# Kernel tuning notes

Measured on AMD Instinct MI355X. Metric: run time of the kernel, lower is better.

Reference implementation:

```python
import jax, jax.numpy as jnp
import numpy as np

N = 10000   # total nodes (hits) across events
K = 16      # n_neighbours (excluding self)
F = 64      # input feature dim
H = 128     # hidden width (hard-coded in module)
BIG = 1e9

def _selu(x):
    return jax.nn.selu(x)

def _glorot(key, shape):
    fan_in, fan_out = shape
    s = jnp.sqrt(2.0 / (fan_in + fan_out)).astype(jnp.float32)
    return jax.random.normal(key, shape, dtype=jnp.float32) * s

def setup_inputs() -> dict:
    key = jax.random.key(0)
    ks = jax.random.split(key, 10)
    h = jax.random.normal(ks[0], (N, F), dtype=jnp.float32)
    coords = jax.random.normal(ks[1], (N, 3), dtype=jnp.float32)
    row_splits = jnp.array([0, N // 2, N], dtype=jnp.int32)
    return {
        'h': h, 'coords': coords, 'row_splits': row_splits,
        'W_e1': _glorot(ks[2], (2 * F + 1, H)), 'b_e1': jnp.zeros((H,), jnp.float32),
        'W_e2': _glorot(ks[3], (H, H)), 'b_e2': jnp.zeros((H,), jnp.float32),
        'W_c1': _glorot(ks[4], (H, H)), 'b_c1': jnp.zeros((H,), jnp.float32),
        'W_c2': _glorot(ks[5], (H, 1)), 'b_c2': jnp.zeros((1,), jnp.float32),
        'W_n1': _glorot(ks[6], (H + F, H)), 'b_n1': jnp.zeros((H,), jnp.float32),
        'W_n2': _glorot(ks[7], (H, H)), 'b_n2': jnp.zeros((H,), jnp.float32),
    }

def _knn(coords, row_splits):
    # segment id per node from row_splits (constant)
    n = coords.shape[0]
    seg = jnp.searchsorted(row_splits, jnp.arange(n), side='right') - 1
    nrm = jnp.sum(coords * coords, axis=1)                      # [N]
    d2 = nrm[:, None] + nrm[None, :] - 2.0 * (coords @ coords.T)
    d2 = jnp.maximum(d2, 0.0)
    same = seg[:, None] == seg[None, :]
    d2 = jnp.where(same, d2, BIG)
    negd, idx = jax.lax.top_k(-d2, K + 1)                       # includes self (dist 0)
    dist = jnp.maximum(-negd, 0.0)                              # [N, K+1]
    return idx, dist

def reference(h, coords, row_splits, W_e1, b_e1, W_e2, b_e2, W_c1, b_c1, W_c2, b_c2, W_n1, b_n1, W_n2, b_n2):
    idx, dist = _knn(coords, row_splits)                        # [N,K+1]
    nidx = idx[:, 1:]                                           # [N,K]
    d = dist[:, 1:]                                             # [N,K]
    coord_diff = coords[:, None, :] - coords[idx[:, 1:]]        # [N,K,3]

    hg = h[idx]                                                 # SelectWithDefault gather [N,K+1,F]
    h_self = hg[:, 0, :]                                        # [N,F]
    h_node = jnp.broadcast_to(h_self[:, None, :], (h.shape[0], K, F)).reshape(-1, F)
    h_neig = hg[:, 1:, :].reshape(-1, F)
    radial0 = d.reshape(-1, 1)

    e = jnp.concatenate([radial0, h_node, h_neig], axis=1)      # [N*K, 2F+1]
    e = _selu(e @ W_e1 + b_e1)
    e = _selu(e @ W_e2 + b_e2)                                  # [N*K, H]

    c = _selu(e @ W_c1 + b_c1)
    w = (c @ W_c2 + b_c2).reshape(-1, K, 1)                     # [N,K,1]
    trans = jnp.mean(coord_diff * w, axis=1)                    # [N,3]
    coords_new = coords + trans

    e_sum = e.reshape(-1, K, H).sum(axis=1)                     # [N,H]
    agg = jnp.concatenate([e_sum, h_self], axis=1)              # [N,H+F]
    out = _selu(agg @ W_n1 + b_n1) @ W_n2 + b_n2                # [N,H]
    return out, coords_new, nidx, d
```

## Files before the change

kernel.cpp:

```cpp
#include <hip/hip_runtime.h>
#include <cstdint>

#define KNB 16
#define FDIM 64
#define HDIM 128
#define SA 130
#define SW 65
#define CMAXW 80

typedef unsigned long long ull;
typedef _Float16 f16x8 __attribute__((ext_vector_type(8)));
typedef float    f32x16 __attribute__((ext_vector_type(16)));

__device__ __forceinline__ float selu_f(float x){
    const float a = 1.6732632423543772f, s = 1.0507009873554805f;
    return x > 0.f ? s * x : s * a * expm1f(x);
}

__device__ __forceinline__ unsigned int pack2(float a, float b){
    union { _Float16 h[2]; unsigned int u; } t;
    t.h[0] = (_Float16)a; t.h[1] = (_Float16)b;
    return t.u;
}

__device__ __forceinline__ f16x8 ldfrag(const unsigned int* p, unsigned int di){
    union { unsigned int u[4]; f16x8 v; } t;
    t.u[0] = p[di]; t.u[1] = p[di+1]; t.u[2] = p[di+2]; t.u[3] = p[di+3];
    return t.v;
}

template<int CTRL>
__device__ __forceinline__ unsigned int dppmin_u32(unsigned int v){
    unsigned int t = (unsigned int)__builtin_amdgcn_update_dpp(
        -1, (int)v, CTRL, 0xF, 0xF, false);
    return t < v ? t : v;
}
__device__ __forceinline__ unsigned int wave_min_u32(unsigned int v){
    v = dppmin_u32<0x111>(v);
    v = dppmin_u32<0x112>(v);
    v = dppmin_u32<0x114>(v);
    v = dppmin_u32<0x118>(v);
    v = dppmin_u32<0x142>(v);
    v = dppmin_u32<0x143>(v);
    return (unsigned int)__builtin_amdgcn_readlane((int)v, 63);
}

__global__ __launch_bounds__(256) void conv_kernel(
    const float* __restrict__ We1, const float* __restrict__ We2,
    const float* __restrict__ Wc1, _Float16* __restrict__ WT)
{
    int id = blockIdx.x * 256 + threadIdx.x;
    int m  = id >> 14;
    int r  = id & 16383;
    int nn = (r >> 7) & 127;
    int k  = r & 127;
    float v;
    if (m == 0)      v = We1[(k + 1) * 128 + nn];
    else if (m == 1) v = We2[k * 128 + nn];
    else             v = Wc1[k * 128 + nn];
    WT[m * 16384 + nn * 128 + k] = (_Float16)v;
}

__global__ __launch_bounds__(256) void knn_kernel(
    const float* __restrict__ coords,
    const int* __restrict__ row_splits, int nseg, int n,
    int* __restrict__ nidx, float* __restrict__ ndist, int* __restrict__ idx0,
    float* __restrict__ out_nidx, float* __restrict__ out_d)
{
    const int lane = threadIdx.x & 63;
    const int wid  = threadIdx.x >> 6;
    const int i    = blockIdx.x * 4 + wid;
    if (i >= n) return;

    int lo = 0, hi = n;
    for (int s = 0; s < nseg; ++s){
        int a = row_splits[s], b = row_splits[s+1];
        if (i >= a && i < b){ lo = a; hi = b; }
    }

    const float cx = coords[3*i], cy = coords[3*i+1], cz = coords[3*i+2];
    const float nrmi = __fadd_rn(__fadd_rn(__fmul_rn(cx,cx), __fmul_rn(cy,cy)), __fmul_rn(cz,cz));

    const int jbase = lo + lane;
    const float FINF = __uint_as_float(0x7f800000u);

    ull m1 = ~0ull, m2 = ~0ull, m3 = ~0ull;
    {
        const float* cp = coords + (size_t)3 * jbase;
        for (int c = 0; c < CMAXW; ++c){
            int j = jbase + c*64;
            float dv = FINF;
            if (j < hi){
                float x = cp[0], y = cp[1], z = cp[2];
                float nrmj = __fadd_rn(__fadd_rn(__fmul_rn(x,x), __fmul_rn(y,y)), __fmul_rn(z,z));
                float dot  = __fadd_rn(__fadd_rn(__fmul_rn(cx,x), __fmul_rn(cy,y)), __fmul_rn(cz,z));
                float d2 = __fsub_rn(__fadd_rn(nrmi, nrmj), __fmul_rn(2.0f, dot));
                dv = fmaxf(d2, 0.0f);
            }
            cp += 192;
            ull kk = (((ull)__float_as_uint(dv)) << 32) | (unsigned int)j;
            ull n1 = kk < m1 ? kk : m1;
            ull t1 = kk < m1 ? m1 : kk;
            ull n2 = t1 < m2 ? t1 : m2;
            ull t2 = t1 < m2 ? m2 : t1;
            ull n3 = t2 < m3 ? t2 : m3;
            m1 = n1; m2 = n2; m3 = n3;
        }
    }
    int vcnt = 3;

    for (int r = 0; r < KNB + 1; ++r){
        unsigned int h32 = (unsigned int)(m1 >> 32);
        unsigned int l32 = (unsigned int)m1;
        unsigned int wmd = wave_min_u32(h32);
        unsigned int jm  = (h32 == wmd) ? l32 : 0xFFFFFFFFu;
        unsigned int wmj = wave_min_u32(jm);

        bool own = (h32 == wmd) && (l32 == wmj);
        bool need = false;
        if (own){
            int   j  = (int)wmj;
            float dv = __uint_as_float(wmd);
            if (r == 0){
                idx0[i] = j;
            } else {
                int rr = r - 1;
                nidx[i*KNB + rr]     = j;
                ndist[i*KNB + rr]    = dv;
                out_nidx[i*KNB + rr] = (float)j;
                out_d[i*KNB + rr]    = dv;
            }
            m1 = m2; m2 = m3; m3 = ~0ull;
            need = (--vcnt == 0);
        }

        if (__ballot((int)need)){
            if (need){
                ull b = (((ull)wmd) << 32) | wmj;
                m1 = m2 = m3 = ~0ull;
                const float* cq = coords + (size_t)3 * jbase;
                for (int c = 0; c < CMAXW; ++c){
                    int j = jbase + c*64;
                    float dv = FINF;
                    if (j < hi){
                        float x = cq[0], y = cq[1], z = cq[2];
                        float nrmj = __fadd_rn(__fadd_rn(__fmul_rn(x,x), __fmul_rn(y,y)), __fmul_rn(z,z));
                        float dot  = __fadd_rn(__fadd_rn(__fmul_rn(cx,x), __fmul_rn(cy,y)), __fmul_rn(cz,z));
                        float d2 = __fsub_rn(__fadd_rn(nrmi, nrmj), __fmul_rn(2.0f, dot));
                        dv = fmaxf(d2, 0.0f);
                    }
                    cq += 192;
                    ull kk = (((ull)__float_as_uint(dv)) << 32) | (unsigned int)j;
                    kk = kk > b ? kk : ~0ull;
                    ull n1 = kk < m1 ? kk : m1;
                    ull t1 = kk < m1 ? m1 : kk;
                    ull n2 = t1 < m2 ? t1 : m2;
                    ull t2 = t1 < m2 ? m2 : t1;
                    ull n3 = t2 < m3 ? t2 : m3;
                    m1 = n1; m2 = n2; m3 = n3;
                }
                vcnt = 3;
            }
        }
    }
}

__global__ __launch_bounds__(256, 3) void egcn_node_kernel(
    const float* __restrict__ h, const float* __restrict__ coords,
    const int* __restrict__ nidx, const float* __restrict__ ndist,
    const int* __restrict__ idx0, const _Float16* __restrict__ WTg,
    const float* __restrict__ W_e1, const float* __restrict__ b_e1,
    const float* __restrict__ b_e2, const float* __restrict__ b_c1,
    const float* __restrict__ W_c2, const float* __restrict__ b_c2,
    float* __restrict__ aggout, float* __restrict__ out_coords, int n)
{
    __shared__ _Float16 Act[64 * SA];
    __shared__ unsigned int wt[128 * SW];
    __shared__ float agg[4][HDIM];
    __shared__ float dls[64];
    __shared__ int   nb[64];
    __shared__ int   j0s[4];
    __shared__ float wedge[64];
    __shared__ float wedgep[2][64];

    const int g0  = blockIdx.x * 4;
    const int tid = threadIdx.x;
    const int lane = tid & 63, wid = tid >> 6;
    const int ln31 = lane & 31, grp = lane >> 5;
    const int rt  = wid & 1;
    const int ct0 = (wid >> 1) * 2;

    if (tid < 64){
        int e = min(g0*KNB + tid, n*KNB - 1);
        nb[tid]  = nidx[e];
        dls[tid] = ndist[e];
    }
    if (tid < 4) j0s[tid] = idx0[min(g0 + tid, n - 1)];
    __syncthreads();

    unsigned int* actd = (unsigned int*)Act;

    {
        int r = tid >> 2, q = tid & 3, f0 = q * 16;
        const float* hs = h + (size_t)j0s[r >> 4] * FDIM + f0;
        const float* hn = h + (size_t)nb[r] * FDIM + f0;
        unsigned int ds = (unsigned int)(r * SA + f0) >> 1;
        unsigned int dn = (unsigned int)(r * SA + FDIM + f0) >> 1;
        #pragma unroll
        for (int j = 0; j < 8; ++j){
            actd[ds + j] = pack2(hs[2*j], hs[2*j+1]);
            actd[dn + j] = pack2(hn[2*j], hn[2*j+1]);
        }
    }
    {
        int nr = tid >> 1, kh = (tid & 1) * 64;
        const uint4* src = (const uint4*)(WTg + nr * 128 + kh);
        unsigned int* dst = wt + nr * SW + (tid & 1) * 32;
        #pragma unroll
        for (int j = 0; j < 8; ++j){
            uint4 x = src[j];
            dst[j*4+0]=x.x; dst[j*4+1]=x.y; dst[j*4+2]=x.z; dst[j*4+3]=x.w;
        }
    }
    __syncthreads();

    const unsigned int aBase  = (unsigned int)(rt*32 + ln31) * SW + grp*4;
    const unsigned int bBase0 = (unsigned int)(ct0*32 + ln31) * SW + grp*4;
    const unsigned int bBase1 = (unsigned int)((ct0+1)*32 + ln31) * SW + grp*4;

    auto gemm2 = [&](f32x16& A0, f32x16& A1){
        #pragma unroll
        for (int ks = 0; ks < 8; ++ks){
            const unsigned int off = ks * 8;
            f16x8 af  = ldfrag(actd, aBase + off);
            f16x8 bf0 = ldfrag(wt, bBase0 + off);
            f16x8 bf1 = ldfrag(wt, bBase1 + off);
            A0 = __builtin_amdgcn_mfma_f32_32x32x16_f16(af, bf0, A0, 0, 0, 0);
            A1 = __builtin_amdgcn_mfma_f32_32x32x16_f16(af, bf1, A1, 0, 0, 0);
        }
    };
    auto stage_wt = [&](const _Float16* Wg){
        int nr = tid >> 1, kh = (tid & 1) * 64;
        const uint4* src = (const uint4*)(Wg + nr * 128 + kh);
        unsigned int* dst = wt + nr * SW + (tid & 1) * 32;
        #pragma unroll
        for (int j = 0; j < 8; ++j){
            uint4 x = src[j];
            dst[j*4+0]=x.x; dst[j*4+1]=x.y; dst[j*4+2]=x.z; dst[j*4+3]=x.w;
        }
    };

    {
        float w0a = W_e1[ct0*32 + ln31], w0b = W_e1[(ct0+1)*32 + ln31];
        float bza = b_e1[ct0*32 + ln31], bzb = b_e1[(ct0+1)*32 + ln31];
        f32x16 a0, a1;
        #pragma unroll
        for (int reg = 0; reg < 16; ++reg){
            int row32 = (reg&3) + 8*(reg>>2) + 4*grp;
            float dv = dls[rt*32 + row32];
            a0[reg] = fmaf(dv, w0a, bza);
            a1[reg] = fmaf(dv, w0b, bzb);
        }
        gemm2(a0, a1);
        __syncthreads();
        #pragma unroll
        for (int reg = 0; reg < 16; ++reg){
            int row = rt*32 + (reg&3) + 8*(reg>>2) + 4*grp;
            Act[row*SA + ct0*32 + ln31]     = (_Float16)selu_f(a0[reg]);
            Act[row*SA + (ct0+1)*32 + ln31] = (_Float16)selu_f(a1[reg]);
        }
        stage_wt(WTg + 16384);
        __syncthreads();
    }

    {
        float bza = b_e2[ct0*32 + ln31], bzb = b_e2[(ct0+1)*32 + ln31];
        f32x16 a0, a1;
        #pragma unroll
        for (int reg = 0; reg < 16; ++reg){ a0[reg] = bza; a1[reg] = bzb; }
        gemm2(a0, a1);
        __syncthreads();
        float ev0[16], ev1[16];
        float slo0 = 0.f, shi0 = 0.f, slo1 = 0.f, shi1 = 0.f;
        #pragma unroll
        for (int reg = 0; reg < 16; ++reg){
            ev0[reg] = selu_f(a0[reg]);
            ev1[reg] = selu_f(a1[reg]);
            if (reg < 8){ slo0 += ev0[reg]; slo1 += ev1[reg]; }
            else        { shi0 += ev0[reg]; shi1 += ev1[reg]; }
        }
        slo0 += __shfl_xor(slo0, 32, 64);
        shi0 += __shfl_xor(shi0, 32, 64);
        slo1 += __shfl_xor(slo1, 32, 64);
        shi1 += __shfl_xor(shi1, 32, 64);
        if (grp == 0){
            agg[rt*2+0][ct0*32 + ln31]     = slo0;
            agg[rt*2+1][ct0*32 + ln31]     = shi0;
            agg[rt*2+0][(ct0+1)*32 + ln31] = slo1;
            agg[rt*2+1][(ct0+1)*32 + ln31] = shi1;
        }
        #pragma unroll
        for (int reg = 0; reg < 16; ++reg){
            int row = rt*32 + (reg&3) + 8*(reg>>2) + 4*grp;
            Act[row*SA + ct0*32 + ln31]     = (_Float16)ev0[reg];
            Act[row*SA + (ct0+1)*32 + ln31] = (_Float16)ev1[reg];
        }
        stage_wt(WTg + 2*16384);
        __syncthreads();
    }

    {
        float bza = b_c1[ct0*32 + ln31], bzb = b_c1[(ct0+1)*32 + ln31];
        f32x16 a0, a1;
        #pragma unroll
        for (int reg = 0; reg < 16; ++reg){ a0[reg] = bza; a1[reg] = bzb; }
        gemm2(a0, a1);
        __syncthreads();
        float wca = W_c2[ct0*32 + ln31], wcb = W_c2[(ct0+1)*32 + ln31];
        float p[16];
        #pragma unroll
        for (int reg = 0; reg < 16; ++reg)
            p[reg] = selu_f(a0[reg]) * wca + selu_f(a1[reg]) * wcb;
        #pragma unroll
        for (int msk = 16; msk > 0; msk >>= 1){
            #pragma unroll
            for (int reg = 0; reg < 16; ++reg)
                p[reg] += __shfl_xor(p[reg], msk, 64);
        }
        if (ln31 == 0){
            #pragma unroll
            for (int reg = 0; reg < 16; ++reg){
                int row = rt*32 + (reg&3) + 8*(reg>>2) + 4*grp;
                wedgep[wid>>1][row] = p[reg];
            }
        }
        __syncthreads();
    }

    if (tid < 64) wedge[tid] = b_c2[0] + wedgep[0][tid] + wedgep[1][tid];
    __syncthreads();

    if (tid < 12){
        int nd = tid / 3, c = tid - nd*3;
        int gi = min(g0 + nd, n - 1);
        float ci = coords[3*gi + c];
        float s = 0.f;
        #pragma unroll
        for (int k = 0; k < KNB; ++k){
            int e = nd*KNB + k;
            s += (ci - coords[3*nb[e] + c]) * wedge[e];
        }
        if (g0 + nd < n) out_coords[3*gi + c] = ci + s * (1.0f/KNB);
    }

    for (int s = tid; s < 4*192; s += 256){
        int nd = s / 192, c = s - nd*192;
        if (g0 + nd < n){
            float v = (c < HDIM) ? agg[nd][c]
                                 : h[(size_t)j0s[nd]*FDIM + (c - HDIM)];
            aggout[(size_t)(g0 + nd)*192 + c] = v;
        }
    }
}

#define NMB 16
__global__ __launch_bounds__(256) void node_mlp_kernel(
    const float* __restrict__ aggin,
    const float* __restrict__ W_n1, const float* __restrict__ b_n1,
    const float* __restrict__ W_n2, const float* __restrict__ b_n2,
    float* __restrict__ out, int n)
{
    __shared__ __attribute__((aligned(16))) float sinT[192][20];
    __shared__ float part[2][NMB][HDIM];

    const int g0  = blockIdx.x * NMB;
    const int tid = threadIdx.x;
    const int o    = tid & 127;
    const int half = tid >> 7;

    for (int s = tid; s < NMB*192; s += 256){
        size_t gidx = (size_t)g0*192 + s;
        size_t lim  = (size_t)n*192 - 1;
        float v = aggin[gidx < lim ? gidx : lim];
        int nd = s / 192, in = s - nd*192;
        sinT[in][nd] = v;
    }
    __syncthreads();

    {
        float a[NMB];
        #pragma unroll
        for (int d = 0; d < NMB; ++d) a[d] = 0.f;
        int in0 = half * 96;
        for (int in = in0; in < in0 + 96; ++in){
            float w = W_n1[in*HDIM + o];
            const float4* sp = (const float4*)&sinT[in][0];
            float4 v0 = sp[0], v1 = sp[1], v2 = sp[2], v3 = sp[3];
            a[0]  = fmaf(v0.x, w, a[0]);  a[1]  = fmaf(v0.y, w, a[1]);
            a[2]  = fmaf(v0.z, w, a[2]);  a[3]  = fmaf(v0.w, w, a[3]);
            a[4]  = fmaf(v1.x, w, a[4]);  a[5]  = fmaf(v1.y, w, a[5]);
            a[6]  = fmaf(v1.z, w, a[6]);  a[7]  = fmaf(v1.w, w, a[7]);
            a[8]  = fmaf(v2.x, w, a[8]);  a[9]  = fmaf(v2.y, w, a[9]);
            a[10] = fmaf(v2.z, w, a[10]); a[11] = fmaf(v2.w, w, a[11]);
            a[12] = fmaf(v3.x, w, a[12]); a[13] = fmaf(v3.y, w, a[13]);
            a[14] = fmaf(v3.z, w, a[14]); a[15] = fmaf(v3.w, w, a[15]);
        }
        #pragma unroll
        for (int d = 0; d < NMB; ++d) part[half][d][o] = a[d];
    }
    __syncthreads();

    for (int s = tid; s < NMB*HDIM; s += 256){
        int nd = s >> 7, o2 = s & 127;
        sinT[o2][nd] = selu_f(part[0][nd][o2] + part[1][nd][o2] + b_n1[o2]);
    }
    __syncthreads();

    {
        float a[NMB];
        #pragma unroll
        for (int d = 0; d < NMB; ++d) a[d] = 0.f;
        int in0 = half * 64;
        for (int in = in0; in < in0 + 64; ++in){
            float w = W_n2[in*HDIM + o];
            const float4* sp = (const float4*)&sinT[in][0];
            float4 v0 = sp[0], v1 = sp[1], v2 = sp[2], v3 = sp[3];
            a[0]  = fmaf(v0.x, w, a[0]);  a[1]  = fmaf(v0.y, w, a[1]);
            a[2]  = fmaf(v0.z, w, a[2]);  a[3]  = fmaf(v0.w, w, a[3]);
            a[4]  = fmaf(v1.x, w, a[4]);  a[5]  = fmaf(v1.y, w, a[5]);
            a[6]  = fmaf(v1.z, w, a[6]);  a[7]  = fmaf(v1.w, w, a[7]);
            a[8]  = fmaf(v2.x, w, a[8]);  a[9]  = fmaf(v2.y, w, a[9]);
            a[10] = fmaf(v2.z, w, a[10]); a[11] = fmaf(v2.w, w, a[11]);
            a[12] = fmaf(v3.x, w, a[12]); a[13] = fmaf(v3.y, w, a[13]);
            a[14] = fmaf(v3.z, w, a[14]); a[15] = fmaf(v3.w, w, a[15]);
        }
        #pragma unroll
        for (int d = 0; d < NMB; ++d) part[half][d][o] = a[d];
    }
    __syncthreads();

    for (int s = tid; s < NMB*HDIM; s += 256){
        int nd = s >> 7, o2 = s & 127;
        if (g0 + nd < n)
            out[(size_t)(g0 + nd)*HDIM + o2] =
                part[0][nd][o2] + part[1][nd][o2] + b_n2[o2];
    }
}

extern "C" void kernel_launch(void* const* d_in, const int* in_sizes, int n_in,
                              void* d_out, int out_size, void* d_ws, size_t ws_size,
                              hipStream_t stream)
{
    const float* h          = (const float*)d_in[0];
    const float* coords     = (const float*)d_in[1];
    const int*   row_splits = (const int*)  d_in[2];
    const float* W_e1 = (const float*)d_in[3];
    const float* b_e1 = (const float*)d_in[4];
    const float* W_e2 = (const float*)d_in[5];
    const float* b_e2 = (const float*)d_in[6];
    const float* W_c1 = (const float*)d_in[7];
    const float* b_c1 = (const float*)d_in[8];
    const float* W_c2 = (const float*)d_in[9];
    const float* b_c2 = (const float*)d_in[10];
    const float* W_n1 = (const float*)d_in[11];
    const float* b_n1 = (const float*)d_in[12];
    const float* W_n2 = (const float*)d_in[13];
    const float* b_n2 = (const float*)d_in[14];

    const int n    = in_sizes[0] / FDIM;
    const int nseg = in_sizes[2] - 1;

    float* out        = (float*)d_out;
    float* out_coords = out + (size_t)n * HDIM;
    float* out_nidx   = out_coords + (size_t)n * 3;
    float* out_d      = out_nidx + (size_t)n * KNB;

    int*       nidx_i = (int*)d_ws;
    float*     ndist  = (float*)(nidx_i + (size_t)n * KNB);
    int*       idx0   = (int*)(ndist + (size_t)n * KNB);
    _Float16*  WT     = (_Float16*)(idx0 + (size_t)n);
    float*     aggbuf = (float*)(WT + 3 * 16384);

    conv_kernel<<<192, 256, 0, stream>>>(W_e1, W_e2, W_c1, WT);

    knn_kernel<<<(n + 3) / 4, 256, 0, stream>>>(coords, row_splits, nseg, n,
                                                nidx_i, ndist, idx0, out_nidx, out_d);

    egcn_node_kernel<<<(n + 3) / 4, 256, 0, stream>>>(
        h, coords, nidx_i, ndist, idx0, WT,
        W_e1, b_e1, b_e2, b_c1, W_c2, b_c2,
        aggbuf, out_coords, n);

    node_mlp_kernel<<<(n + NMB - 1) / NMB, 256, 0, stream>>>(
        aggbuf, W_n1, b_n1, W_n2, b_n2, out, n);
}
```

Measured before the change: 285.7 us.

## Pack coords as float4, unroll KNN scan, double edge tile per block

A new pre-pass packs coordinates together with their squared norm into float4, so the KNN scan does one vector load per candidate and skips recomputing the norm. The scan's first pass is unrolled by four to overlap loads. The edge MLP kernel now handles 8 nodes (128 edge rows) per block, with each wave computing all four 32-column tiles. Fragment loads use 128-bit LDS reads with padded strides, and selu switches to __expf. Shared memory per block grows and occupancy drops to 2 blocks per CU, and the fast exp may slightly change precision.

After: 257.7 us. 1.11x faster.

```diff
diff --git a/kernel.cpp b/kernel.cpp
--- a/kernel.cpp
+++ b/kernel.cpp
@@ -4,8 +4,11 @@
 #define KNB 16
 #define FDIM 64
 #define HDIM 128
-#define SA 130
-#define SW 65
+#define NPB 8
+#define ROWS 128
+#define SA 136
+#define SAD 68
+#define SW 68
 #define CMAXW 80
 
 typedef unsigned long long ull;
@@ -14,7 +17,7 @@
 
 __device__ __forceinline__ float selu_f(float x){
     const float a = 1.6732632423543772f, s = 1.0507009873554805f;
-    return x > 0.f ? s * x : s * a * expm1f(x);
+    return x > 0.f ? s * x : s * a * (__expf(x) - 1.0f);
 }
 
 __device__ __forceinline__ unsigned int pack2(float a, float b){
@@ -23,9 +26,9 @@
     return t.u;
 }
 
-__device__ __forceinline__ f16x8 ldfrag(const unsigned int* p, unsigned int di){
-    union { unsigned int u[4]; f16x8 v; } t;
-    t.u[0] = p[di]; t.u[1] = p[di+1]; t.u[2] = p[di+2]; t.u[3] = p[di+3];
+__device__ __forceinline__ f16x8 ldfrag4(const unsigned int* p, unsigned int di){
+    union { uint4 q; f16x8 v; } t;
+    t.q = *(const uint4*)(p + di);
     return t.v;
 }
 
@@ -61,8 +64,19 @@
     WT[m * 16384 + nn * 128 + k] = (_Float16)v;
 }
 
+__global__ __launch_bounds__(256) void pack4_kernel(
+    const float* __restrict__ coords, float4* __restrict__ c4, int n)
+{
+    int i = blockIdx.x * 256 + threadIdx.x;
+    if (i < n){
+        float x = coords[3*i], y = coords[3*i+1], z = coords[3*i+2];
+        float nrm = __fadd_rn(__fadd_rn(__fmul_rn(x,x), __fmul_rn(y,y)), __fmul_rn(z,z));
+        c4[i] = make_float4(x, y, z, nrm);
+    }
+}
+
 __global__ __launch_bounds__(256) void knn_kernel(
-    const float* __restrict__ coords,
+    const float4* __restrict__ c4,
     const int* __restrict__ row_splits, int nseg, int n,
     int* __restrict__ nidx, float* __restrict__ ndist, int* __restrict__ idx0,
     float* __restrict__ out_nidx, float* __restrict__ out_d)
@@ -78,34 +92,42 @@
         if (i >= a && i < b){ lo = a; hi = b; }
     }
 
-    const float cx = coords[3*i], cy = coords[3*i+1], cz = coords[3*i+2];
-    const float nrmi = __fadd_rn(__fadd_rn(__fmul_rn(cx,cx), __fmul_rn(cy,cy)), __fmul_rn(cz,cz));
+    const float4 ci = c4[i];
+    const float cx = ci.x, cy = ci.y, cz = ci.z, nrmi = ci.w;
 
     const int jbase = lo + lane;
     const float FINF = __uint_as_float(0x7f800000u);
 
     ull m1 = ~0ull, m2 = ~0ull, m3 = ~0ull;
-    {
-        const float* cp = coords + (size_t)3 * jbase;
-        for (int c = 0; c < CMAXW; ++c){
-            int j = jbase + c*64;
-            float dv = FINF;
-            if (j < hi){
-                float x = cp[0], y = cp[1], z = cp[2];
-                float nrmj = __fadd_rn(__fadd_rn(__fmul_rn(x,x), __fmul_rn(y,y)), __fmul_rn(z,z));
-                float dot  = __fadd_rn(__fadd_rn(__fmul_rn(cx,x), __fmul_rn(cy,y)), __fmul_rn(cz,z));
-                float d2 = __fsub_rn(__fadd_rn(nrmi, nrmj), __fmul_rn(2.0f, dot));
-                dv = fmaxf(d2, 0.0f);
-            }
-            cp += 192;
-            ull kk = (((ull)__float_as_uint(dv)) << 32) | (unsigned int)j;
-            ull n1 = kk < m1 ? kk : m1;
-            ull t1 = kk < m1 ? m1 : kk;
-            ull n2 = t1 < m2 ? t1 : m2;
-            ull t2 = t1 < m2 ? m2 : t1;
-            ull n3 = t2 < m3 ? t2 : m3;
-            m1 = n1; m2 = n2; m3 = n3;
-        }
+
+    #define D2_OF(v) __fsub_rn(__fadd_rn(nrmi, (v).w), __fmul_rn(2.0f, \
+        __fadd_rn(__fadd_rn(__fmul_rn(cx,(v).x), __fmul_rn(cy,(v).y)), __fmul_rn(cz,(v).z))))
+    #define INS(kk) { \
+        ull n1 = (kk) < m1 ? (kk) : m1; \
+        ull t1 = (kk) < m1 ? m1 : (kk); \
+        ull n2 = t1 < m2 ? t1 : m2; \
+        ull t2 = t1 < m2 ? m2 : t1; \
+        ull n3 = t2 < m3 ? t2 : m3; \
+        m1 = n1; m2 = n2; m3 = n3; }
+
+    for (int c0 = 0; c0 < CMAXW; c0 += 4){
+        int j0 = jbase + (c0+0)*64;
+        int j1 = jbase + (c0+1)*64;
+        int j2 = jbase + (c0+2)*64;
+        int j3 = jbase + (c0+3)*64;
+        float4 v0 = c4[min(j0, hi-1)];
+        float4 v1 = c4[min(j1, hi-1)];
+        float4 v2 = c4[min(j2, hi-1)];
+        float4 v3 = c4[min(j3, hi-1)];
+        float d0 = (j0 < hi) ? fmaxf(D2_OF(v0), 0.0f) : FINF;
+        float d1 = (j1 < hi) ? fmaxf(D2_OF(v1), 0.0f) : FINF;
+        float d2 = (j2 < hi) ? fmaxf(D2_OF(v2), 0.0f) : FINF;
+        float d3 = (j3 < hi) ? fmaxf(D2_OF(v3), 0.0f) : FINF;
+        ull k0 = (((ull)__float_as_uint(d0)) << 32) | (unsigned int)j0;
+        ull k1 = (((ull)__float_as_uint(d1)) << 32) | (unsigned int)j1;
+        ull k2 = (((ull)__float_as_uint(d2)) << 32) | (unsigned int)j2;
+        ull k3 = (((ull)__float_as_uint(d3)) << 32) | (unsigned int)j3;
+        INS(k0) INS(k1) INS(k2) INS(k3)
     }
     int vcnt = 3;
 
@@ -138,34 +160,23 @@
             if (need){
                 ull b = (((ull)wmd) << 32) | wmj;
                 m1 = m2 = m3 = ~0ull;
-                const float* cq = coords + (size_t)3 * jbase;
                 for (int c = 0; c < CMAXW; ++c){
                     int j = jbase + c*64;
-                    float dv = FINF;
-                    if (j < hi){
-                        float x = cq[0], y = cq[1], z = cq[2];
-                        float nrmj = __fadd_rn(__fadd_rn(__fmul_rn(x,x), __fmul_rn(y,y)), __fmul_rn(z,z));
-                        float dot  = __fadd_rn(__fadd_rn(__fmul_rn(cx,x), __fmul_rn(cy,y)), __fmul_rn(cz,z));
-                        float d2 = __fsub_rn(__fadd_rn(nrmi, nrmj), __fmul_rn(2.0f, dot));
-                        dv = fmaxf(d2, 0.0f);
-                    }
-                    cq += 192;
+                    float4 v = c4[min(j, hi-1)];
+                    float dv = (j < hi) ? fmaxf(D2_OF(v), 0.0f) : FINF;
                     ull kk = (((ull)__float_as_uint(dv)) << 32) | (unsigned int)j;
                     kk = kk > b ? kk : ~0ull;
-                    ull n1 = kk < m1 ? kk : m1;
-                    ull t1 = kk < m1 ? m1 : kk;
-                    ull n2 = t1 < m2 ? t1 : m2;
-                    ull t2 = t1 < m2 ? m2 : t1;
-                    ull n3 = t2 < m3 ? t2 : m3;
-                    m1 = n1; m2 = n2; m3 = n3;
+                    INS(kk)
                 }
                 vcnt = 3;
             }
         }
     }
-}
-
-__global__ __launch_bounds__(256, 3) void egcn_node_kernel(
+    #undef INS
+    #undef D2_OF
+}
+
+__global__ __launch_bounds__(256, 2) void egcn_node_kernel(
     const float* __restrict__ h, const float* __restrict__ coords,
     const int* __restrict__ nidx, const float* __restrict__ ndist,
     const int* __restrict__ idx0, const _Float16* __restrict__ WTg,
@@ -174,153 +185,165 @@
     const float* __restrict__ W_c2, const float* __restrict__ b_c2,
     float* __restrict__ aggout, float* __restrict__ out_coords, int n)
 {
-    __shared__ _Float16 Act[64 * SA];
-    __shared__ unsigned int wt[128 * SW];
-    __shared__ float agg[4][HDIM];
-    __shared__ float dls[64];
-    __shared__ int   nb[64];
-    __shared__ int   j0s[4];
-    __shared__ float wedge[64];
-    __shared__ float wedgep[2][64];
-
-    const int g0  = blockIdx.x * 4;
+    __shared__ __attribute__((aligned(16))) _Float16 Act[ROWS * SA];
+    __shared__ __attribute__((aligned(16))) unsigned int wt[ROWS * SW];
+    __shared__ float agg[NPB][HDIM];
+    __shared__ float dls[ROWS];
+    __shared__ int   nb[ROWS];
+    __shared__ int   j0s[NPB];
+    __shared__ float wedge[ROWS];
+
+    const int g0  = blockIdx.x * NPB;
     const int tid = threadIdx.x;
     const int lane = tid & 63, wid = tid >> 6;
     const int ln31 = lane & 31, grp = lane >> 5;
-    const int rt  = wid & 1;
-    const int ct0 = (wid >> 1) * 2;
-
-    if (tid < 64){
+    const int rt  = wid;
+
+    if (tid < ROWS){
         int e = min(g0*KNB + tid, n*KNB - 1);
         nb[tid]  = nidx[e];
         dls[tid] = ndist[e];
     }
-    if (tid < 4) j0s[tid] = idx0[min(g0 + tid, n - 1)];
+    if (tid < NPB) j0s[tid] = idx0[min(g0 + tid, n - 1)];
     __syncthreads();
 
     unsigned int* actd = (unsigned int*)Act;
 
     {
-        int r = tid >> 2, q = tid & 3, f0 = q * 16;
-        const float* hs = h + (size_t)j0s[r >> 4] * FDIM + f0;
-        const float* hn = h + (size_t)nb[r] * FDIM + f0;
-        unsigned int ds = (unsigned int)(r * SA + f0) >> 1;
-        unsigned int dn = (unsigned int)(r * SA + FDIM + f0) >> 1;
-        #pragma unroll
-        for (int j = 0; j < 8; ++j){
-            actd[ds + j] = pack2(hs[2*j], hs[2*j+1]);
-            actd[dn + j] = pack2(hn[2*j], hn[2*j+1]);
-        }
-    }
-    {
-        int nr = tid >> 1, kh = (tid & 1) * 64;
-        const uint4* src = (const uint4*)(WTg + nr * 128 + kh);
-        unsigned int* dst = wt + nr * SW + (tid & 1) * 32;
-        #pragma unroll
-        for (int j = 0; j < 8; ++j){
-            uint4 x = src[j];
-            dst[j*4+0]=x.x; dst[j*4+1]=x.y; dst[j*4+2]=x.z; dst[j*4+3]=x.w;
-        }
-    }
+        int r = tid >> 1, half = tid & 1;
+        const float4* hs = (const float4*)(h + (size_t)j0s[r >> 4] * FDIM + half*32);
+        const float4* hn = (const float4*)(h + (size_t)nb[r] * FDIM + half*32);
+        unsigned int base = (unsigned int)r * SAD + half*16;
+        uint4 buf[4];
+        #pragma unroll
+        for (int q = 0; q < 4; ++q){
+            float4 a = hs[2*q], b = hs[2*q+1];
+            buf[q].x = pack2(a.x,a.y); buf[q].y = pack2(a.z,a.w);
+            buf[q].z = pack2(b.x,b.y); buf[q].w = pack2(b.z,b.w);
+        }
+        #pragma unroll
+        for (int q = 0; q < 4; ++q) *(uint4*)(actd + base + 4*q) = buf[q];
+        #pragma unroll
+        for (int q = 0; q < 4; ++q){
+            float4 a = hn[2*q], b = hn[2*q+1];
+            buf[q].x = pack2(a.x,a.y); buf[q].y = pack2(a.z,a.w);
+            buf[q].z = pack2(b.x,b.y); buf[q].w = pack2(b.z,b.w);
+        }
+        #pragma unroll
+        for (int q = 0; q < 4; ++q) *(uint4*)(actd + base + 32 + 4*q) = buf[q];
+    }
+    auto stage_wt = [&](const _Float16* Wg){
+        int nr = tid >> 1, half = tid & 1;
+        const uint4* src = (const uint4*)(Wg + nr * 128 + half*64);
+        uint4* dst = (uint4*)(wt + nr * SW + half*32);
+        #pragma unroll
+        for (int q = 0; q < 8; ++q) dst[q] = src[q];
+    };
+    stage_wt(WTg);
     __syncthreads();
 
-    const unsigned int aBase  = (unsigned int)(rt*32 + ln31) * SW + grp*4;
-    const unsigned int bBase0 = (unsigned int)(ct0*32 + ln31) * SW + grp*4;
-    const unsigned int bBase1 = (unsigned int)((ct0+1)*32 + ln31) * SW + grp*4;
-
-    auto gemm2 = [&](f32x16& A0, f32x16& A1){
+    const unsigned int aBase = (unsigned int)(rt*32 + ln31) * SAD + grp*4;
+    const unsigned int bB0   = (unsigned int)(ln31      ) * SW + grp*4;
+    const unsigned int bB1   = (unsigned int)(32  + ln31) * SW + grp*4;
+    const unsigned int bB2   = (unsigned int)(64  + ln31) * SW + grp*4;
+    const unsigned int bB3   = (unsigned int)(96  + ln31) * SW + grp*4;
+
+    auto gemm4 = [&](f32x16& A0, f32x16& A1, f32x16& A2, f32x16& A3){
         #pragma unroll
         for (int ks = 0; ks < 8; ++ks){
             const unsigned int off = ks * 8;
-            f16x8 af  = ldfrag(actd, aBase + off);
-            f16x8 bf0 = ldfrag(wt, bBase0 + off);
-            f16x8 bf1 = ldfrag(wt, bBase1 + off);
-            A0 = __builtin_amdgcn_mfma_f32_32x32x16_f16(af, bf0, A0, 0, 0, 0);
-            A1 = __builtin_amdgcn_mfma_f32_32x32x16_f16(af, bf1, A1, 0, 0, 0);
+            f16x8 af = ldfrag4(actd, aBase + off);
+            A0 = __builtin_amdgcn_mfma_f32_32x32x16_f16(af, ldfrag4(wt, bB0 + off), A0, 0, 0, 0);
+            A1 = __builtin_amdgcn_mfma_f32_32x32x16_f16(af, ldfrag4(wt, bB1 + off), A1, 0, 0, 0);
+            A2 = __builtin_amdgcn_mfma_f32_32x32x16_f16(af, ldfrag4(wt, bB2 + off), A2, 0, 0, 0);
+            A3 = __builtin_amdgcn_mfma_f32_32x32x16_f16(af, ldfrag4(wt, bB3 + off), A3, 0, 0, 0);
         }
     };
-    auto stage_wt = [&](const _Float16* Wg){
-        int nr = tid >> 1, kh = (tid & 1) * 64;
-        const uint4* src = (const uint4*)(Wg + nr * 128 + kh);
-        unsigned int* dst = wt + nr * SW + (tid & 1) * 32;
-        #pragma unroll
-        for (int j = 0; j < 8; ++j){
-            uint4 x = src[j];
-            dst[j*4+0]=x.x; dst[j*4+1]=x.y; dst[j*4+2]=x.z; dst[j*4+3]=x.w;
-        }
-    };
+    #define ROW_OF(reg) (rt*32 + ((reg)&3) + 8*((reg)>>2) + 4*grp)
 
     {
-        float w0a = W_e1[ct0*32 + ln31], w0b = W_e1[(ct0+1)*32 + ln31];
-        float bza = b_e1[ct0*32 + ln31], bzb = b_e1[(ct0+1)*32 + ln31];
-        f32x16 a0, a1;
+        float w00 = W_e1[ln31],      w01 = W_e1[32+ln31];
+        float w02 = W_e1[64+ln31],   w03 = W_e1[96+ln31];
+        float bz0 = b_e1[ln31],      bz1 = b_e1[32+ln31];
+        float bz2 = b_e1[64+ln31],   bz3 = b_e1[96+ln31];
+        f32x16 a0, a1, a2, a3;
         #pragma unroll
         for (int reg = 0; reg < 16; ++reg){
-            int row32 = (reg&3) + 8*(reg>>2) + 4*grp;
-            float dv = dls[rt*32 + row32];
-            a0[reg] = fmaf(dv, w0a, bza);
-            a1[reg] = fmaf(dv, w0b, bzb);
-        }
-        gemm2(a0, a1);
+            float dv = dls[ROW_OF(reg)];
+            a0[reg] = fmaf(dv, w00, bz0);
+            a1[reg] = fmaf(dv, w01, bz1);
+            a2[reg] = fmaf(dv, w02, bz2);
+            a3[reg] = fmaf(dv, w03, bz3);
+        }
+        gemm4(a0, a1, a2, a3);
         __syncthreads();
         #pragma unroll
         for (int reg = 0; reg < 16; ++reg){
-            int row = rt*32 + (reg&3) + 8*(reg>>2) + 4*grp;
-            Act[row*SA + ct0*32 + ln31]     = (_Float16)selu_f(a0[reg]);
-            Act[row*SA + (ct0+1)*32 + ln31] = (_Float16)selu_f(a1[reg]);
+            int row = ROW_OF(reg);
+            Act[row*SA + ln31]      = (_Float16)selu_f(a0[reg]);
+            Act[row*SA + 32 + ln31] = (_Float16)selu_f(a1[reg]);
+            Act[row*SA + 64 + ln31] = (_Float16)selu_f(a2[reg]);
+            Act[row*SA + 96 + ln31] = (_Float16)selu_f(a3[reg]);
         }
         stage_wt(WTg + 16384);
         __syncthreads();
     }
 
     {
-        float bza = b_e2[ct0*32 + ln31], bzb = b_e2[(ct0+1)*32 + ln31];
-        f32x16 a0, a1;
-        #pragma unroll
-        for (int reg = 0; reg < 16; ++reg){ a0[reg] = bza; a1[reg] = bzb; }
-        gemm2(a0, a1);
+        float bz0 = b_e2[ln31],    bz1 = b_e2[32+ln31];
+        float bz2 = b_e2[64+ln31], bz3 = b_e2[96+ln31];
+        f32x16 a0, a1, a2, a3;
+        #pragma unroll
+        for (int reg = 0; reg < 16; ++reg){ a0[reg]=bz0; a1[reg]=bz1; a2[reg]=bz2; a3[reg]=bz3; }
+        gemm4(a0, a1, a2, a3);
         __syncthreads();
-        float ev0[16], ev1[16];
-        float slo0 = 0.f, shi0 = 0.f, slo1 = 0.f, shi1 = 0.f;
+        float e0[16], e1v[16], e2v[16], e3[16];
+        float sl0=0.f, sh0=0.f, sl1=0.f, sh1=0.f, sl2=0.f, sh2=0.f, sl3=0.f, sh3=0.f;
         #pragma unroll
         for (int reg = 0; reg < 16; ++reg){
-            ev0[reg] = selu_f(a0[reg]);
-            ev1[reg] = selu_f(a1[reg]);
-            if (reg < 8){ slo0 += ev0[reg]; slo1 += ev1[reg]; }
-            else        { shi0 += ev0[reg]; shi1 += ev1[reg]; }
-        }
-        slo0 += __shfl_xor(slo0, 32, 64);
-        shi0 += __shfl_xor(shi0, 32, 64);
-        slo1 += __shfl_xor(slo1, 32, 64);
-        shi1 += __shfl_xor(shi1, 32, 64);
+            e0[reg]=selu_f(a0[reg]); e1v[reg]=selu_f(a1[reg]);
+            e2v[reg]=selu_f(a2[reg]); e3[reg]=selu_f(a3[reg]);
+            if (reg < 8){ sl0+=e0[reg]; sl1+=e1v[reg]; sl2+=e2v[reg]; sl3+=e3[reg]; }
+            else        { sh0+=e0[reg]; sh1+=e1v[reg]; sh2+=e2v[reg]; sh3+=e3[reg]; }
+        }
+        sl0 += __shfl_xor(sl0, 32, 64);  sh0 += __shfl_xor(sh0, 32, 64);
+        sl1 += __shfl_xor(sl1, 32, 64);  sh1 += __shfl_xor(sh1, 32, 64);
+        sl2 += __shfl_xor(sl2, 32, 64);  sh2 += __shfl_xor(sh2, 32, 64);
+        sl3 += __shfl_xor(sl3, 32, 64);  sh3 += __shfl_xor(sh3, 32, 64);
         if (grp == 0){
-            agg[rt*2+0][ct0*32 + ln31]     = slo0;
-            agg[rt*2+1][ct0*32 + ln31]     = shi0;
-            agg[rt*2+0][(ct0+1)*32 + ln31] = slo1;
-            agg[rt*2+1][(ct0+1)*32 + ln31] = shi1;
+            agg[rt*2+0][ln31]      = sl0;  agg[rt*2+1][ln31]      = sh0;
+            agg[rt*2+0][32 + ln31] = sl1;  agg[rt*2+1][32 + ln31] = sh1;
+            agg[rt*2+0][64 + ln31] = sl2;  agg[rt*2+1][64 + ln31] = sh2;
+            agg[rt*2+0][96 + ln31] = sl3;  agg[rt*2+1][96 + ln31] = sh3;
         }
         #pragma unroll
         for (int reg = 0; reg < 16; ++reg){
-            int row = rt*32 + (reg&3) + 8*(reg>>2) + 4*grp;
-            Act[row*SA + ct0*32 + ln31]     = (_Float16)ev0[reg];
-            Act[row*SA + (ct0+1)*32 + ln31] = (_Float16)ev1[reg];
+            int row = ROW_OF(reg);
+            Act[row*SA + ln31]      = (_Float16)e0[reg];
+            Act[row*SA + 32 + ln31] = (_Float16)e1v[reg];
+            Act[row*SA + 64 + ln31] = (_Float16)e2v[reg];
+            Act[row*SA + 96 + ln31] = (_Float16)e3[reg];
         }
         stage_wt(WTg + 2*16384);
         __syncthreads();
     }
 
     {
-        float bza = b_c1[ct0*32 + ln31], bzb = b_c1[(ct0+1)*32 + ln31];
-        f32x16 a0, a1;
-        #pragma unroll
-        for (int reg = 0; reg < 16; ++reg){ a0[reg] = bza; a1[reg] = bzb; }
-        gemm2(a0, a1);
+        float bz0 = b_c1[ln31],    bz1 = b_c1[32+ln31];
+        float bz2 = b_c1[64+ln31], bz3 = b_c1[96+ln31];
+        f32x16 a0, a1, a2, a3;
+        #pragma unroll
+        for (int reg = 0; reg < 16; ++reg){ a0[reg]=bz0; a1[reg]=bz1; a2[reg]=bz2; a3[reg]=bz3; }
+        gemm4(a0, a1, a2, a3);
         __syncthreads();
-        float wca = W_c2[ct0*32 + ln31], wcb = W_c2[(ct0+1)*32 + ln31];
+        float wc0 = W_c2[ln31],    wc1 = W_c2[32+ln31];
+        float wc2 = W_c2[64+ln31], wc3 = W_c2[96+ln31];
+        float bc2 = b_c2[0];
         float p[16];
         #pragma unroll
         for (int reg = 0; reg < 16; ++reg)
-            p[reg] = selu_f(a0[reg]) * wca + selu_f(a1[reg]) * wcb;
+            p[reg] = selu_f(a0[reg])*wc0 + selu_f(a1[reg])*wc1
+                   + selu_f(a2[reg])*wc2 + selu_f(a3[reg])*wc3;
         #pragma unroll
         for (int msk = 16; msk > 0; msk >>= 1){
             #pragma unroll
@@ -329,18 +352,13 @@
         }
         if (ln31 == 0){
             #pragma unroll
-            for (int reg = 0; reg < 16; ++reg){
-                int row = rt*32 + (reg&3) + 8*(reg>>2) + 4*grp;
-                wedgep[wid>>1][row] = p[reg];
-            }
+            for (int reg = 0; reg < 16; ++reg)
+                wedge[ROW_OF(reg)] = bc2 + p[reg];
         }
         __syncthreads();
     }
 
-    if (tid < 64) wedge[tid] = b_c2[0] + wedgep[0][tid] + wedgep[1][tid];
-    __syncthreads();
-
-    if (tid < 12){
+    if (tid < 3*NPB){
         int nd = tid / 3, c = tid - nd*3;
         int gi = min(g0 + nd, n - 1);
         float ci = coords[3*gi + c];
@@ -353,7 +371,7 @@
         if (g0 + nd < n) out_coords[3*gi + c] = ci + s * (1.0f/KNB);
     }
 
-    for (int s = tid; s < 4*192; s += 256){
+    for (int s = tid; s < NPB*192; s += 256){
         int nd = s / 192, c = s - nd*192;
         if (g0 + nd < n){
             float v = (c < HDIM) ? agg[nd][c]
@@ -480,13 +498,15 @@
     int*       idx0   = (int*)(ndist + (size_t)n * KNB);
     _Float16*  WT     = (_Float16*)(idx0 + (size_t)n);
     float*     aggbuf = (float*)(WT + 3 * 16384);
+    float4*    c4     = (float4*)(aggbuf + (size_t)n * 192);
 
     conv_kernel<<<192, 256, 0, stream>>>(W_e1, W_e2, W_c1, WT);
-
-    knn_kernel<<<(n + 3) / 4, 256, 0, stream>>>(coords, row_splits, nseg, n,
+    pack4_kernel<<<(n + 255) / 256, 256, 0, stream>>>(coords, c4, n);
+
+    knn_kernel<<<(n + 3) / 4, 256, 0, stream>>>(c4, row_splits, nseg, n,
                                                 nidx_i, ndist, idx0, out_nidx, out_d);
 
-    egcn_node_kernel<<<(n + 3) / 4, 256, 0, stream>>>(
+    egcn_node_kernel<<<(n + NPB - 1) / NPB, 256, 0, stream>>>(
         h, coords, nidx_i, ndist, idx0, WT,
         W_e1, b_e1, b_e2, b_c1, W_c2, b_c2,
         aggbuf, out_coords, n);
```
